# Optimization experiments

Measured on AMD Instinct MI355X. Metric: run time of the kernel, lower is better.

Reference implementation:

```python
import jax, jax.numpy as jnp
import numpy as np

B, S, DIN = 2, 2048, 2048
H, G, D = 32, 8, 64  # num_heads, num_kv_groups, head_dim
GS = H // G          # group_size
EPS = 1e-6


def _rmsnorm(x, scale):
    # qwen3-compatible: compute in fp32, cast back
    xf = x.astype(jnp.float32)
    ms = jnp.mean(xf * xf, axis=-1, keepdims=True)
    return (xf * jax.lax.rsqrt(ms + EPS) * scale).astype(x.dtype)


def _rope(x, cos, sin):
    # x: [b, h, s, d]; cos/sin: [s, d]
    d2 = x.shape[-1] // 2
    x1, x2 = x[..., :d2], x[..., d2:]
    rotated = jnp.concatenate([-x2, x1], axis=-1)
    return (x * cos[None, None] + rotated * sin[None, None]).astype(x.dtype)


def setup_inputs() -> dict:
    key = jax.random.key(0)
    ks = jax.random.split(key, 8)
    x = jax.random.normal(ks[0], (B, S, DIN), dtype=jnp.float32)
    # causal mask: True = masked (future positions)
    mask = jnp.triu(jnp.ones((S, S), dtype=bool), k=1)
    # standard RoPE tables [S, D]
    inv_freq = 1.0 / (10000.0 ** (np.arange(0, D, 2, dtype=np.float32) / D))
    ang = np.arange(S, dtype=np.float32)[:, None] * inv_freq[None, :]
    ang = np.concatenate([ang, ang], axis=-1)  # [S, D]
    cos = jnp.asarray(np.cos(ang), dtype=jnp.float32)
    sin = jnp.asarray(np.sin(ang), dtype=jnp.float32)
    s = 0.02
    Wq = jax.random.normal(ks[1], (DIN, H * D), dtype=jnp.float32) * s
    Wk = jax.random.normal(ks[2], (DIN, G * D), dtype=jnp.float32) * s
    Wv = jax.random.normal(ks[3], (DIN, G * D), dtype=jnp.float32) * s
    Wo = jax.random.normal(ks[4], (H * D, DIN), dtype=jnp.float32) * s
    q_scale = jnp.ones((D,), dtype=jnp.float32)
    k_scale = jnp.ones((D,), dtype=jnp.float32)
    return dict(x=x, mask=mask, cos=cos, sin=sin, Wq=Wq, Wk=Wk, Wv=Wv, Wo=Wo,
                q_scale=q_scale, k_scale=k_scale)


def reference(x, mask, cos, sin, Wq, Wk, Wv, Wo, q_scale, k_scale):
    b, s, _ = x.shape
    # QKV projections -> [b, heads, s, D]
    q = (x @ Wq).reshape(b, s, H, D).transpose(0, 2, 1, 3)
    k = (x @ Wk).reshape(b, s, G, D).transpose(0, 2, 1, 3)
    v = (x @ Wv).reshape(b, s, G, D).transpose(0, 2, 1, 3)
    # qk RMSNorm (per-head-dim)
    q = _rmsnorm(q, q_scale)
    k = _rmsnorm(k, k_scale)
    # RoPE (start_pos=0, no cache)
    q = _rope(q, cos, sin)
    k = _rope(k, cos, sin)
    # GQA: group query heads instead of repeat_interleaving KV (same math)
    qg = q.reshape(b, G, GS, s, D)
    scores = jnp.einsum('bghqd,bgkd->bghqk', qg, k) / jnp.float32(np.sqrt(D))
    scores = jnp.where(mask[None, None, None], -jnp.inf, scores)
    w = jax.nn.softmax(scores, axis=-1)
    ctx = jnp.einsum('bghqk,bgkd->bghqd', w, v)
    ctx = ctx.reshape(b, H, s, D).transpose(0, 2, 1, 3).reshape(b, s, H * D)
    out = ctx @ Wo
    return out, (k, v)
```

## Files before the change

### kernel.cpp

```cpp
#include <hip/hip_runtime.h>

typedef __bf16 bf16_t;
typedef bf16_t bf16x8 __attribute__((ext_vector_type(8)));
typedef float f32x4 __attribute__((ext_vector_type(4)));

#define MFMA16(a, b, c) __builtin_amdgcn_mfma_f32_16x16x32_bf16(a, b, c, 0, 0, 0)

__device__ __forceinline__ unsigned short f2bf(float f) {
    union { float f; unsigned u; } v; v.f = f;
    unsigned r = v.u + 0x7FFFu + ((v.u >> 16) & 1u);
    return (unsigned short)(r >> 16);
}
__device__ __forceinline__ float bf2f(unsigned short h) {
    union { unsigned u; float f; } v; v.u = ((unsigned)h) << 16;
    return v.f;
}
__device__ __forceinline__ unsigned short to_bf(float f) {
    bf16_t b = (bf16_t)f;
    return __builtin_bit_cast(unsigned short, b);
}

__device__ __forceinline__ void gll16(const unsigned short* g, unsigned short* l) {
    __builtin_amdgcn_global_load_lds(
        (const __attribute__((address_space(1))) unsigned int*)g,
        (__attribute__((address_space(3))) unsigned int*)l, 16, 0, 0);
}

__global__ __launch_bounds__(256) void cast_x_kernel(const float* __restrict__ src,
                                                     unsigned short* __restrict__ dst, int n) {
    int i = (blockIdx.x * 256 + threadIdx.x) * 4;
    if (i >= n) return;
    float4 v = *(const float4*)&src[i];
    union { unsigned short e[4]; uint2 u; } p;
    p.e[0] = f2bf(v.x); p.e[1] = f2bf(v.y); p.e[2] = f2bf(v.z); p.e[3] = f2bf(v.w);
    *(uint2*)&dst[i] = p.u;
}

__global__ __launch_bounds__(256) void castT_kernel(const float* __restrict__ src,
                                                    unsigned short* __restrict__ dst,
                                                    int N) {
    __shared__ __align__(16) unsigned short sT[64 * 68];
    int nt = blockIdx.x >> 5;
    int kt = blockIdx.x & 31;
    int k0 = kt * 64, n0 = nt * 64;
    int t = threadIdx.x;
#pragma unroll
    for (int c = t; c < 1024; c += 256) {
        int r = c >> 4, c4 = c & 15;
        float4 v = *(const float4*)&src[(size_t)(k0 + r) * N + n0 + c4 * 4];
        union { unsigned short e[4]; uint2 u; } p;
        p.e[0] = f2bf(v.x); p.e[1] = f2bf(v.y); p.e[2] = f2bf(v.z); p.e[3] = f2bf(v.w);
        *(uint2*)&sT[r * 68 + c4 * 4] = p.u;
    }
    __syncthreads();
#pragma unroll
    for (int c = t; c < 512; c += 256) {
        int n = c >> 3, cb = c & 7;
        union { unsigned short e[8]; uint4 v; } u;
#pragma unroll
        for (int j = 0; j < 8; ++j) u.e[j] = sT[(cb * 8 + j) * 68 + n];
        *(uint4*)&dst[(size_t)(n0 + n) * 2048 + k0 + cb * 8] = u.v;
    }
}

__global__ __launch_bounds__(256) void gemm_bt(
    const unsigned short* __restrict__ A,
    const unsigned short* __restrict__ Bt,
    float* __restrict__ Cf, unsigned short* __restrict__ Cb,
    int M, int N, int K)
{
    __shared__ __align__(16) unsigned short sA[128 * 64];
    __shared__ __align__(16) unsigned short sB[128 * 64];
    int n0 = blockIdx.x * 128, m0 = blockIdx.y * 128;
    int tid = threadIdx.x;
    int lane = tid & 63, w = tid >> 6;
    int wm = (w >> 1) * 64, wn = (w & 1) * 64;
    int lo = lane & 15, quad = lane >> 4;

    int srow = w * 32 + (lane >> 3);
    int scol = (lane & 7) * 8;
    const unsigned short* Ag = &A[(size_t)(m0 + srow) * K + scol];
    const unsigned short* Bg = &Bt[(size_t)(n0 + srow) * K + scol];

    f32x4 acc[4][4];
#pragma unroll
    for (int i = 0; i < 4; ++i)
#pragma unroll
        for (int j = 0; j < 4; ++j) acc[i][j] = (f32x4){0.f, 0.f, 0.f, 0.f};

    for (int kt = 0; kt < K; kt += 64) {
#pragma unroll
        for (int c = 0; c < 4; ++c) {
            gll16(Ag + (size_t)(c * 8) * K + kt, &sA[(w * 4 + c) * 512]);
            gll16(Bg + (size_t)(c * 8) * K + kt, &sB[(w * 4 + c) * 512]);
        }
        __syncthreads();
#pragma unroll
        for (int ks = 0; ks < 64; ks += 32) {
            bf16x8 af[4], bfr[4];
#pragma unroll
            for (int mi = 0; mi < 4; ++mi)
                af[mi] = *(const bf16x8*)&sA[(wm + mi * 16 + lo) * 64 + ks + quad * 8];
#pragma unroll
            for (int ni = 0; ni < 4; ++ni)
                bfr[ni] = *(const bf16x8*)&sB[(wn + ni * 16 + lo) * 64 + ks + quad * 8];
#pragma unroll
            for (int mi = 0; mi < 4; ++mi)
#pragma unroll
                for (int ni = 0; ni < 4; ++ni)
                    acc[mi][ni] = MFMA16(af[mi], bfr[ni], acc[mi][ni]);
        }
        __syncthreads();
    }

#pragma unroll
    for (int mi = 0; mi < 4; ++mi)
#pragma unroll
        for (int ni = 0; ni < 4; ++ni)
#pragma unroll
            for (int r = 0; r < 4; ++r) {
                int row = m0 + wm + mi * 16 + quad * 4 + r;
                int col = n0 + wn + ni * 16 + lo;
                if (Cf) Cf[(size_t)row * N + col] = acc[mi][ni][r];
                else    Cb[(size_t)row * N + col] = f2bf(acc[mi][ni][r]);
            }
}

__global__ __launch_bounds__(256) void rmsrope_kernel(
    const unsigned short* __restrict__ qkv,
    const float* __restrict__ cosb, const float* __restrict__ sinb,
    const float* __restrict__ q_scale, const float* __restrict__ k_scale,
    unsigned short* __restrict__ q_attn, unsigned short* __restrict__ k_attn,
    float* __restrict__ k_out, float* __restrict__ v_out)
{
    int wid = blockIdx.x * 4 + (threadIdx.x >> 6);
    int lane = threadIdx.x & 63;
    int t = wid % 48;
    int bs = wid / 48;
    int b = bs >> 11, s = bs & 2047;

    if (t >= 40) {
        int g = t - 40;
        float val = bf2f(qkv[(size_t)bs * 3072 + 2560 + g * 64 + lane]);
        v_out[(size_t)((b * 8 + g) * 2048 + s) * 64 + lane] = val;
        return;
    }
    bool is_q = (t < 32);
    int col = is_q ? (t * 64) : (2048 + (t - 32) * 64);
    float val = bf2f(qkv[(size_t)bs * 3072 + col + lane]);
    float ss = val * val;
#pragma unroll
    for (int m = 1; m < 64; m <<= 1) ss += __shfl_xor(ss, m);
    float rs = rsqrtf(ss * (1.0f / 64.0f) + 1e-6f);
    float scl = is_q ? q_scale[lane] : k_scale[lane];
    float xn = val * rs * scl;
    float other = __shfl_xor(xn, 32);
    float rot = (lane < 32) ? -other : other;
    float o = xn * cosb[s * 64 + lane] + rot * sinb[s * 64 + lane];
    if (is_q) {
        q_attn[(size_t)((b * 32 + t) * 2048 + s) * 64 + lane] = to_bf(o * (0.125f * 1.44269504f));
    } else {
        int g = t - 32;
        size_t idx = (size_t)((b * 8 + g) * 2048 + s) * 64 + lane;
        k_attn[idx] = to_bf(o);
        k_out[idx] = o;
    }
}

__global__ __launch_bounds__(256) void vtrans_kernel(
    const unsigned short* __restrict__ qkv, unsigned short* __restrict__ vt)
{
    __shared__ __align__(16) unsigned short sT[64 * 68];
    int idx = blockIdx.x;
    int st = idx & 31, g = (idx >> 5) & 7, b = idx >> 8;
    int tid = threadIdx.x;
#pragma unroll
    for (int c = tid; c < 512; c += 256) {
        int r = c >> 3, cb = c & 7;
        *(uint4*)&sT[r * 68 + cb * 8] =
            *(const uint4*)&qkv[(size_t)(b * 2048 + st * 64 + r) * 3072 + 2560 + g * 64 + cb * 8];
    }
    __syncthreads();
#pragma unroll
    for (int c = tid; c < 512; c += 256) {
        int d = c >> 3, cb = c & 7;
        union { unsigned short e[8]; uint4 v; } u;
#pragma unroll
        for (int j = 0; j < 8; ++j) u.e[j] = sT[(cb * 8 + j) * 68 + d];
        *(uint4*)&vt[((size_t)(b * 8 + g) * 64 + d) * 2048 + st * 64 + cb * 8] = u.v;
    }
}

__global__ __launch_bounds__(256, 2) void attn_kernel(
    const unsigned short* __restrict__ q_attn,
    const unsigned short* __restrict__ k_attn,
    const unsigned short* __restrict__ vt,
    unsigned short* __restrict__ ctx)
{
    __shared__ __align__(16) unsigned short sK[2][4096];
    __shared__ __align__(16) unsigned short sV[2][4096];
    __shared__ __align__(16) unsigned short sP[4][16 * 68];

    int w = threadIdx.x >> 6;
    int lane = threadIdx.x & 63;

    int g = blockIdx.x & 7;
    int ord = blockIdx.x >> 3;
    int b = ord & 1;
    int qt = 63 - (ord >> 1);
    int h = g * 4 + w;

    int lo = lane & 15, quad = lane >> 4;
    unsigned short* sPw = sP[w];

    const unsigned short* Qb = q_attn + (size_t)(b * 32 + h) * 2048 * 64;
    const unsigned short* Kb = k_attn + (size_t)(b * 8 + g) * 2048 * 64;
    const unsigned short* Vb = vt + (size_t)(b * 8 + g) * 64 * 2048;

    int nt = (qt >> 1) + 1;

    int rsub = lane >> 3;
    int csw  = ((lane & 7) ^ rsub) << 3;

    auto STAGE = [&](int buf, int kt) {
#pragma unroll
        for (int i = 0; i < 2; ++i) {
            int c = w + i * 4;
            gll16(Kb + (size_t)(kt * 64 + c * 8 + rsub) * 64 + csw, &sK[buf][c * 512]);
            gll16(Vb + (size_t)(c * 8 + rsub) * 2048 + kt * 64 + csw, &sV[buf][c * 512]);
        }
    };

    const bf16_t one = (bf16_t)1.0f;
    const bf16x8 vone = {one, one, one, one, one, one, one, one};

    bf16x8 qf[2][2];
#pragma unroll
    for (int mt = 0; mt < 2; ++mt)
#pragma unroll
        for (int h2 = 0; h2 < 2; ++h2)
            qf[mt][h2] = *(const bf16x8*)&Qb[(size_t)(qt * 32 + mt * 16 + lo) * 64 + h2 * 32 + quad * 8];

    f32x4 o_acc[2][4];
    f32x4 l_acc[2];
#pragma unroll
    for (int mt = 0; mt < 2; ++mt) {
        l_acc[mt] = (f32x4){0.f, 0.f, 0.f, 0.f};
#pragma unroll
        for (int j = 0; j < 4; ++j) o_acc[mt][j] = (f32x4){0.f, 0.f, 0.f, 0.f};
    }

    STAGE(0, 0);
    __syncthreads();

    int cur = 0;
    for (int kt = 0; kt < nt; ++kt) {
        if (kt + 1 < nt) STAGE(cur ^ 1, kt + 1);

        const char* sKc = (const char*)sK[cur];
        const char* sVc = (const char*)sV[cur];
        bool domask = (kt == nt - 1);

#pragma unroll
        for (int mt = 0; mt < 2; ++mt) {
            f32x4 sc[4];
            __builtin_amdgcn_s_setprio(1);
#pragma unroll
            for (int ct = 0; ct < 4; ++ct) {
                int krow = ct * 16 + lo;
                int rsw = (krow & 7) << 4;
                bf16x8 kf0 = *(const bf16x8*)(sKc + (krow << 7) + (((quad << 4)) ^ rsw));
                bf16x8 kf1 = *(const bf16x8*)(sKc + (krow << 7) + (((1 << 6) | (quad << 4)) ^ rsw));
                f32x4 z = (f32x4){0.f, 0.f, 0.f, 0.f};
                z = MFMA16(qf[mt][0], kf0, z);
                z = MFMA16(qf[mt][1], kf1, z);
                sc[ct] = z;
            }
            __builtin_amdgcn_s_setprio(0);
            if (domask) {
                int qrow0 = qt * 32 + mt * 16 + quad * 4;
#pragma unroll
                for (int ct = 0; ct < 4; ++ct)
#pragma unroll
                    for (int r = 0; r < 4; ++r)
                        if (kt * 64 + ct * 16 + lo > qrow0 + r) sc[ct][r] = -INFINITY;
            }
#pragma unroll
            for (int ct = 0; ct < 4; ++ct)
#pragma unroll
                for (int r = 0; r < 4; ++r)
                    sc[ct][r] = __builtin_amdgcn_exp2f(sc[ct][r]);

#pragma unroll
            for (int ct = 0; ct < 4; ++ct)
#pragma unroll
                for (int r = 0; r < 4; ++r)
                    sPw[(quad * 4 + r) * 68 + ct * 16 + lo] = to_bf(sc[ct][r]);

            bf16x8 pf0 = *(const bf16x8*)&sPw[lo * 68 + quad * 8];
            bf16x8 pf1 = *(const bf16x8*)&sPw[lo * 68 + 32 + quad * 8];

            __builtin_amdgcn_s_setprio(1);
            l_acc[mt] = MFMA16(pf0, vone, l_acc[mt]);
            l_acc[mt] = MFMA16(pf1, vone, l_acc[mt]);

#pragma unroll
            for (int nt2 = 0; nt2 < 4; ++nt2) {
                int vrow = nt2 * 16 + lo;
                int rsw = (vrow & 7) << 4;
                bf16x8 vf0 = *(const bf16x8*)(sVc + (vrow << 7) + (((quad << 4)) ^ rsw));
                bf16x8 vf1 = *(const bf16x8*)(sVc + (vrow << 7) + (((1 << 6) | (quad << 4)) ^ rsw));
                f32x4 oo = o_acc[mt][nt2];
                oo = MFMA16(pf0, vf0, oo);
                oo = MFMA16(pf1, vf1, oo);
                o_acc[mt][nt2] = oo;
            }
            __builtin_amdgcn_s_setprio(0);
        }

        __syncthreads();
        cur ^= 1;
    }

#pragma unroll
    for (int mt = 0; mt < 2; ++mt)
#pragma unroll
        for (int r = 0; r < 4; ++r) {
            float inv = 1.0f / l_acc[mt][r];
            int row = qt * 32 + mt * 16 + quad * 4 + r;
#pragma unroll
            for (int nt2 = 0; nt2 < 4; ++nt2) {
                size_t oi = ((size_t)(b * 2048 + row)) * 2048 + h * 64 + nt2 * 16 + lo;
                ctx[oi] = to_bf(o_acc[mt][nt2][r] * inv);
            }
        }
}

extern "C" void kernel_launch(void* const* d_in, const int* in_sizes, int n_in,
                              void* d_out, int out_size, void* d_ws, size_t ws_size,
                              hipStream_t stream)
{
    (void)in_sizes; (void)n_in; (void)out_size; (void)ws_size;
    const float* x       = (const float*)d_in[0];
    const float* cosb    = (const float*)d_in[2];
    const float* sinb    = (const float*)d_in[3];
    const float* Wq      = (const float*)d_in[4];
    const float* Wk      = (const float*)d_in[5];
    const float* Wv      = (const float*)d_in[6];
    const float* Wo      = (const float*)d_in[7];
    const float* q_scale = (const float*)d_in[8];
    const float* k_scale = (const float*)d_in[9];

    float* out   = (float*)d_out;
    float* k_out = out + 8388608;
    float* v_out = k_out + 2097152;

    char* ws = (char*)d_ws;
    size_t off = 0;
    auto alloc = [&](size_t bytes) {
        char* p = ws + off; off += (bytes + 255) & ~(size_t)255; return p;
    };
    unsigned short* x_bf   = (unsigned short*)alloc(4096ull * 2048 * 2);
    unsigned short* Wqkvt  = (unsigned short*)alloc(3072ull * 2048 * 2);
    unsigned short* Wot    = (unsigned short*)alloc(2048ull * 2048 * 2);
    unsigned short* qkv    = (unsigned short*)alloc(4096ull * 3072 * 2);
    unsigned short* q_attn = (unsigned short*)alloc(4096ull * 2048 * 2);
    unsigned short* k_attn = (unsigned short*)alloc(2048ull * 2048 * 2);
    unsigned short* vt     = (unsigned short*)alloc(2097152ull * 2);
    unsigned short* ctx    = (unsigned short*)alloc(4096ull * 2048 * 2);

    cast_x_kernel<<<8192, 256, 0, stream>>>(x, x_bf, 8388608);
    castT_kernel<<<1024, 256, 0, stream>>>(Wq, Wqkvt, 2048);
    castT_kernel<<<256, 256, 0, stream>>>(Wk, Wqkvt + 2048ull * 2048, 512);
    castT_kernel<<<256, 256, 0, stream>>>(Wv, Wqkvt + 2560ull * 2048, 512);
    castT_kernel<<<1024, 256, 0, stream>>>(Wo, Wot, 2048);

    gemm_bt<<<dim3(24, 32), 256, 0, stream>>>(x_bf, Wqkvt, nullptr, qkv, 4096, 3072, 2048);

    rmsrope_kernel<<<49152, 256, 0, stream>>>(qkv, cosb, sinb, q_scale, k_scale,
                                              q_attn, k_attn, k_out, v_out);
    vtrans_kernel<<<512, 256, 0, stream>>>(qkv, vt);

    attn_kernel<<<1024, 256, 0, stream>>>(q_attn, k_attn, vt, ctx);

    gemm_bt<<<dim3(16, 32), 256, 0, stream>>>(ctx, Wot, out, nullptr, 4096, 2048, 2048);
}
```

Before: 411.0 us.

## Replace 128x128 GEMM with 256x256 double-buffered, swizzled, 8-wave pipelined GEMM

Swaps the simple 128x128-tile GEMM for a 256x256-tile, 512-thread kernel. It double-buffers K tiles in 128KB of dynamic LDS, XOR-swizzles the LDS layout to avoid bank conflicts, and interleaves async global-to-LDS loads with MFMA quadrants using barriers, setprio and vmcnt waits. The aim is to hide memory latency and raise data reuse per tile in both projection GEMMs. In exchange it launches far fewer blocks (192 and 128 on a large CU count), which can leave CUs idle. It also relies on hand-tuned waitcnt correctness.

New measurement: 396.2 us. 3.6% less time.

```diff
diff --git a/kernel.cpp b/kernel.cpp
--- a/kernel.cpp
+++ b/kernel.cpp
@@ -63,67 +63,132 @@
     }
 }
 
-__global__ __launch_bounds__(256) void gemm_bt(
+__global__ __launch_bounds__(512) void gemm256_bt(
     const unsigned short* __restrict__ A,
     const unsigned short* __restrict__ Bt,
     float* __restrict__ Cf, unsigned short* __restrict__ Cb,
     int M, int N, int K)
 {
-    __shared__ __align__(16) unsigned short sA[128 * 64];
-    __shared__ __align__(16) unsigned short sB[128 * 64];
-    int n0 = blockIdx.x * 128, m0 = blockIdx.y * 128;
+    extern __shared__ unsigned short lds[];
+    const int KT = K >> 6;
+    const int NIT = KT >> 1;
+
     int tid = threadIdx.x;
     int lane = tid & 63, w = tid >> 6;
-    int wm = (w >> 1) * 64, wn = (w & 1) * 64;
+    int wmi = w >> 2, wni = w & 3;
     int lo = lane & 15, quad = lane >> 4;
-
-    int srow = w * 32 + (lane >> 3);
-    int scol = (lane & 7) * 8;
-    const unsigned short* Ag = &A[(size_t)(m0 + srow) * K + scol];
-    const unsigned short* Bg = &Bt[(size_t)(n0 + srow) * K + scol];
-
-    f32x4 acc[4][4];
-#pragma unroll
-    for (int i = 0; i < 4; ++i)
+    int m0 = blockIdx.y * 256, n0 = blockIdx.x * 256;
+
+    int rsub = lane >> 3;
+    int csw  = ((lane & 7) ^ rsub) << 3;
+
+    f32x4 acc[8][4];
+#pragma unroll
+    for (int i = 0; i < 8; ++i)
 #pragma unroll
         for (int j = 0; j < 4; ++j) acc[i][j] = (f32x4){0.f, 0.f, 0.f, 0.f};
 
-    for (int kt = 0; kt < K; kt += 64) {
-#pragma unroll
-        for (int c = 0; c < 4; ++c) {
-            gll16(Ag + (size_t)(c * 8) * K + kt, &sA[(w * 4 + c) * 512]);
-            gll16(Bg + (size_t)(c * 8) * K + kt, &sB[(w * 4 + c) * 512]);
-        }
-        __syncthreads();
-#pragma unroll
-        for (int ks = 0; ks < 64; ks += 32) {
-            bf16x8 af[4], bfr[4];
-#pragma unroll
-            for (int mi = 0; mi < 4; ++mi)
-                af[mi] = *(const bf16x8*)&sA[(wm + mi * 16 + lo) * 64 + ks + quad * 8];
-#pragma unroll
-            for (int ni = 0; ni < 4; ++ni)
-                bfr[ni] = *(const bf16x8*)&sB[(wn + ni * 16 + lo) * 64 + ks + quad * 8];
-#pragma unroll
-            for (int mi = 0; mi < 4; ++mi)
-#pragma unroll
-                for (int ni = 0; ni < 4; ++ni)
-                    acc[mi][ni] = MFMA16(af[mi], bfr[ni], acc[mi][ni]);
-        }
-        __syncthreads();
-    }
-
-#pragma unroll
-    for (int mi = 0; mi < 4; ++mi)
-#pragma unroll
-        for (int ni = 0; ni < 4; ++ni)
+    auto stA = [&](int buf, int mp, int T) {
+#pragma unroll
+        for (int j = 0; j < 2; ++j) {
+            int rr = (w * 2 + j) * 8 + rsub;
+            gll16(A + (size_t)(m0 + mp * 128 + rr) * K + T * 64 + csw,
+                  lds + buf * 32768 + mp * 8192 + (w * 2 + j) * 512);
+        }
+    };
+    auto stB = [&](int buf, int np, int T) {
+#pragma unroll
+        for (int j = 0; j < 2; ++j) {
+            int rr = (w * 2 + j) * 8 + rsub;
+            gll16(Bt + (size_t)(n0 + np * 128 + rr) * K + T * 64 + csw,
+                  lds + buf * 32768 + 16384 + np * 8192 + (w * 2 + j) * 512);
+        }
+    };
+
+    auto phase = [&](int buf, int mp, int np, auto stage, bool drain) {
+        bf16x8 a[4][2], b2[2][2];
+#pragma unroll
+        for (int mf = 0; mf < 4; ++mf)
+#pragma unroll
+            for (int k2 = 0; k2 < 2; ++k2) {
+                int r = mp * 128 + wmi * 64 + mf * 16 + lo;
+                int u = quad + k2 * 4;
+                a[mf][k2] = *(const bf16x8*)&lds[buf * 32768 + r * 64 + ((u ^ (lo & 7)) << 3)];
+            }
+#pragma unroll
+        for (int nf = 0; nf < 2; ++nf)
+#pragma unroll
+            for (int k2 = 0; k2 < 2; ++k2) {
+                int r = np * 128 + wni * 32 + nf * 16 + lo;
+                int u = quad + k2 * 4;
+                b2[nf][k2] = *(const bf16x8*)&lds[buf * 32768 + 16384 + r * 64 + ((u ^ (lo & 7)) << 3)];
+            }
+        stage();
+        __builtin_amdgcn_s_barrier();
+        __builtin_amdgcn_sched_barrier(0);
+        __builtin_amdgcn_s_setprio(1);
+#pragma unroll
+        for (int mf = 0; mf < 4; ++mf)
+#pragma unroll
+            for (int nf = 0; nf < 2; ++nf) {
+                f32x4 z = acc[mp * 4 + mf][np * 2 + nf];
+                z = MFMA16(a[mf][0], b2[nf][0], z);
+                z = MFMA16(a[mf][1], b2[nf][1], z);
+                acc[mp * 4 + mf][np * 2 + nf] = z;
+            }
+        __builtin_amdgcn_s_setprio(0);
+        if (drain) asm volatile("s_waitcnt vmcnt(0)" ::: "memory");
+        else       asm volatile("s_waitcnt vmcnt(6)" ::: "memory");
+        __builtin_amdgcn_s_barrier();
+        __builtin_amdgcn_sched_barrier(0);
+    };
+    auto nop = [&] {};
+
+    stA(0, 0, 0); stB(0, 0, 0); stA(0, 1, 0); stB(0, 1, 0);
+    stA(1, 0, 1); stB(1, 0, 1);
+    asm volatile("s_waitcnt vmcnt(4)" ::: "memory");
+    __builtin_amdgcn_s_barrier();
+    __builtin_amdgcn_sched_barrier(0);
+
+    for (int i = 0; i < NIT - 1; ++i) {
+        int T1 = 2 * i + 1, T2 = 2 * i + 2, T3 = 2 * i + 3;
+        phase(0, 0, 0, [&] { stA(1, 1, T1); }, false);
+        phase(0, 0, 1, [&] { stB(1, 1, T1); }, false);
+        phase(0, 1, 0, [&] { stA(0, 0, T2); }, false);
+        phase(0, 1, 1, [&] { stB(0, 0, T2); }, false);
+        phase(1, 0, 0, [&] { stA(0, 1, T2); }, false);
+        phase(1, 0, 1, [&] { stB(0, 1, T2); }, false);
+        phase(1, 1, 0, [&] { stA(1, 0, T3); }, false);
+        phase(1, 1, 1, [&] { stB(1, 0, T3); }, false);
+    }
+    {
+        int T1 = KT - 1;
+        phase(0, 0, 0, [&] { stA(1, 1, T1); }, false);
+        phase(0, 0, 1, [&] { stB(1, 1, T1); }, true);
+        phase(0, 1, 0, nop, false);
+        phase(0, 1, 1, nop, false);
+        phase(1, 0, 0, nop, false);
+        phase(1, 0, 1, nop, false);
+        phase(1, 1, 0, nop, false);
+        phase(1, 1, 1, nop, false);
+    }
+
+#pragma unroll
+    for (int mi = 0; mi < 8; ++mi) {
+        int mp = mi >> 2, mf = mi & 3;
+        int row_base = m0 + mp * 128 + wmi * 64 + mf * 16 + quad * 4;
+#pragma unroll
+        for (int ni = 0; ni < 4; ++ni) {
+            int np = ni >> 1, nf = ni & 1;
+            int col = n0 + np * 128 + wni * 32 + nf * 16 + lo;
 #pragma unroll
             for (int r = 0; r < 4; ++r) {
-                int row = m0 + wm + mi * 16 + quad * 4 + r;
-                int col = n0 + wn + ni * 16 + lo;
+                int row = row_base + r;
                 if (Cf) Cf[(size_t)row * N + col] = acc[mi][ni][r];
                 else    Cb[(size_t)row * N + col] = f2bf(acc[mi][ni][r]);
             }
+        }
+    }
 }
 
 __global__ __launch_bounds__(256) void rmsrope_kernel(
@@ -355,6 +420,13 @@
     float* k_out = out + 8388608;
     float* v_out = k_out + 2097152;
 
+    static bool attr_done = false;
+    if (!attr_done) {
+        hipFuncSetAttribute((const void*)gemm256_bt,
+                            hipFuncAttributeMaxDynamicSharedMemorySize, 131072);
+        attr_done = true;
+    }
+
     char* ws = (char*)d_ws;
     size_t off = 0;
     auto alloc = [&](size_t bytes) {
@@ -375,7 +447,7 @@
     castT_kernel<<<256, 256, 0, stream>>>(Wv, Wqkvt + 2560ull * 2048, 512);
     castT_kernel<<<1024, 256, 0, stream>>>(Wo, Wot, 2048);
 
-    gemm_bt<<<dim3(24, 32), 256, 0, stream>>>(x_bf, Wqkvt, nullptr, qkv, 4096, 3072, 2048);
+    gemm256_bt<<<dim3(12, 16), 512, 131072, stream>>>(x_bf, Wqkvt, nullptr, qkv, 4096, 3072, 2048);
 
     rmsrope_kernel<<<49152, 256, 0, stream>>>(qkv, cosb, sinb, q_scale, k_scale,
                                               q_attn, k_attn, k_out, v_out);
@@ -383,5 +455,5 @@
 
     attn_kernel<<<1024, 256, 0, stream>>>(q_attn, k_attn, vt, ctx);
 
-    gemm_bt<<<dim3(16, 32), 256, 0, stream>>>(ctx, Wot, out, nullptr, 4096, 2048, 2048);
-}
+    gemm256_bt<<<dim3(8, 16), 512, 131072, stream>>>(ctx, Wot, out, nullptr, 4096, 2048, 2048);
+}
```
